# Kernel tuning notes

Measured on AMD Instinct MI355X. Metric: run time of the kernel, lower is better.

Reference implementation:

```python
import jax, jax.numpy as jnp
import numpy as np

N = 50000       # num nodes
E = 600000      # num edges
IN = 128        # in_channels
H = 4           # heads
C = 32          # out_channels per head
B = 3           # num bends (Bezier control points)
NEG_SLOPE = 0.2


def setup_inputs() -> dict:
    key = jax.random.key(0)
    ks = jax.random.split(key, 6)
    x = jax.random.normal(ks[0], (N, IN), dtype=jnp.float32)
    edge_index = jax.random.randint(ks[1], (2, E), 0, N)
    # Bezier coefficients at t=0.5 for a 3-point curve: [0.25, 0.5, 0.25]
    coeffs_t = jnp.array([0.25, 0.5, 0.25], dtype=jnp.float32)
    glorot_w = float(np.sqrt(2.0) * np.sqrt(6.0 / (H * C + IN)))
    glorot_a = float(np.sqrt(2.0) * np.sqrt(6.0 / (1 + C)))
    lin_weight = jax.random.uniform(ks[2], (B, H * C, IN), jnp.float32, -glorot_w, glorot_w)
    lin_bias = jnp.zeros((B, H * C), dtype=jnp.float32)
    att_src = jax.random.uniform(ks[3], (B, 1, H, C), jnp.float32, -glorot_a, glorot_a)
    att_dst = jax.random.uniform(ks[4], (B, 1, H, C), jnp.float32, -glorot_a, glorot_a)
    return {"x": x, "edge_index": edge_index, "coeffs_t": coeffs_t,
            "lin_weight": lin_weight, "lin_bias": lin_bias,
            "att_src": att_src, "att_dst": att_dst}


def reference(x, edge_index, coeffs_t, lin_weight, lin_bias, att_src, att_dst):
    # Bezier parameter interpolation: weighted sum over bends
    W = jnp.einsum('b,boi->oi', coeffs_t, lin_weight)      # [H*C, IN]
    bias = jnp.einsum('b,bo->o', coeffs_t, lin_bias)       # [H*C]
    a_src = jnp.einsum('b,bqhc->qhc', coeffs_t, att_src)   # [1,H,C]
    a_dst = jnp.einsum('b,bqhc->qhc', coeffs_t, att_dst)   # [1,H,C]

    n = x.shape[0]
    xt = (x @ W.T + bias).reshape(n, H, C)                 # [N,H,C]
    alpha_src = jnp.sum(xt * a_src, axis=-1)               # [N,H]
    alpha_dst = jnp.sum(xt * a_dst, axis=-1)               # [N,H]

    row, col = edge_index[0], edge_index[1]
    alpha = alpha_src[row] + alpha_dst[col]                # [E,H]
    alpha = jax.nn.leaky_relu(alpha, NEG_SLOPE)

    # scatter-softmax over incoming edges of each target node (col)
    amax = jax.ops.segment_max(alpha, col, num_segments=n)  # [N,H]
    ex = jnp.exp(alpha - amax[col])                         # [E,H]
    denom = jax.ops.segment_sum(ex, col, num_segments=n)    # [N,H]
    alpha = ex / (denom[col] + 1e-16)                       # [E,H]

    # weighted neighbor aggregation (edge-parallel segment reduction)
    msg = xt[row] * alpha[..., None]                        # [E,H,C]
    out = jax.ops.segment_sum(msg, col, num_segments=n)     # [N,H,C]
    return out.reshape(n, H * C)                            # concat=True
```

## Files before the change

### kernel.cpp

```cpp
#include <hip/hip_runtime.h>
#include <hip/hip_bf16.h>

#define GAT_IN   128
#define GAT_OUT  128
#define GAT_H    4
#define GAT_C    32
#define NEG_SLOPE 0.2f
#define BUCKET   48

typedef __attribute__((ext_vector_type(8))) short bf16x8;
typedef __attribute__((ext_vector_type(4))) float f32x4;
union U4 { uint4 u; bf16x8 v; };

static __device__ __forceinline__ unsigned int pack_bf16(float lo, float hi) {
    __hip_bfloat16 a = __float2bfloat16(lo);
    __hip_bfloat16 b = __float2bfloat16(hi);
    unsigned short ua = *reinterpret_cast<unsigned short*>(&a);
    unsigned short ub = *reinterpret_cast<unsigned short*>(&b);
    return (unsigned int)ua | ((unsigned int)ub << 16);
}

__global__ __launch_bounds__(256) void bucket_interp_kernel(
    const int* __restrict__ ei, int* __restrict__ cnt,
    unsigned short* __restrict__ esrc, int ne,
    const float* __restrict__ coeffs,
    const float* __restrict__ lw,
    const float* __restrict__ lb,
    const float* __restrict__ asr,
    const float* __restrict__ ads,
    unsigned int* __restrict__ wfrag,
    float* __restrict__ biasc,
    float* __restrict__ asrc, float* __restrict__ adst)
{
    int b = blockIdx.x;
    if (b < 32) {
        int i = b * 256 + threadIdx.x;
        float c0 = coeffs[0], c1 = coeffs[1], c2 = coeffs[2];
        int lane = (i >> 2) & 63;
        int nk   = i >> 8;
        int jw   = i & 3;
        int nt = nk >> 2, ks = nk & 3;
        int o = nt * 16 + (lane & 15);
        int k = ks * 32 + (lane >> 4) * 8 + jw * 2;
        int idx = o * 128 + k;
        float w0 = c0 * lw[idx]     + c1 * lw[16384 + idx]     + c2 * lw[32768 + idx];
        float w1 = c0 * lw[idx + 1] + c1 * lw[16384 + idx + 1] + c2 * lw[32768 + idx + 1];
        wfrag[i] = pack_bf16(w0, w1);
        if (b == 0 && threadIdx.x < 128) {
            int t = threadIdx.x;
            biasc[t] = c0 * lb[t]  + c1 * lb[128 + t]  + c2 * lb[256 + t];
            asrc[t]  = c0 * asr[t] + c1 * asr[128 + t] + c2 * asr[256 + t];
            adst[t]  = c0 * ads[t] + c1 * ads[128 + t] + c2 * ads[256 + t];
        }
        return;
    }
    int e = (b - 32) * 256 + threadIdx.x;
    if (e >= ne) return;
    int row = ei[e], col = ei[ne + e];
    int pos = atomicAdd(&cnt[col], 1);
    if (pos < BUCKET)
        esrc[(unsigned)col * BUCKET + pos] = (unsigned short)row;
}

__global__ __launch_bounds__(256) void gemm_alpha_kernel(
    const float* __restrict__ x,
    const unsigned int* __restrict__ wfrag,
    const float* __restrict__ biasc,
    const float* __restrict__ asrc,
    const float* __restrict__ adst,
    unsigned int* __restrict__ xtb,
    float* __restrict__ alpha_src,
    float* __restrict__ alpha_dst,
    int n)
{
    __shared__ __align__(16) float C[64 * 132];
    int tid  = threadIdx.x;
    int lane = tid & 63;
    int wave = tid >> 6;
    int quad = lane >> 4;
    int lm   = lane & 15;
    int m0   = blockIdx.x * 64 + wave * 16;

    f32x4 acc[8];
    #pragma unroll
    for (int t = 0; t < 8; ++t) acc[t] = (f32x4){0.f, 0.f, 0.f, 0.f};

    int arow = m0 + lm; if (arow >= n) arow = n - 1;
    const float4* xr = (const float4*)(x + (size_t)arow * 128 + quad * 8);
    const uint4*  wf = (const uint4*)wfrag;

    #pragma unroll
    for (int ks = 0; ks < 4; ++ks) {
        float4 a0 = xr[ks * 8 + 0];
        float4 a1 = xr[ks * 8 + 1];
        U4 af;
        af.u.x = pack_bf16(a0.x, a0.y);
        af.u.y = pack_bf16(a0.z, a0.w);
        af.u.z = pack_bf16(a1.x, a1.y);
        af.u.w = pack_bf16(a1.z, a1.w);
        #pragma unroll
        for (int nt = 0; nt < 8; ++nt) {
            U4 bf; bf.u = wf[(nt * 4 + ks) * 64 + lane];
            acc[nt] = __builtin_amdgcn_mfma_f32_16x16x32_bf16(
                af.v, bf.v, acc[nt], 0, 0, 0);
        }
    }

    #pragma unroll
    for (int nt = 0; nt < 8; ++nt) {
        int col = nt * 16 + lm;
        #pragma unroll
        for (int r = 0; r < 4; ++r) {
            int rowl = wave * 16 + quad * 4 + r;
            C[rowl * 132 + col] = acc[nt][r];
        }
    }
    __syncthreads();

    int rowl = wave * 16 + (lane >> 2);
    int seg  = lane & 3;
    int mrow = blockIdx.x * 64 + rowl;
    if (mrow < n) {
        const float4* cb = (const float4*)(C + rowl * 132 + seg * 32);
        const float4* bb = (const float4*)(biasc + seg * 32);
        const float4* sb = (const float4*)(asrc + seg * 32);
        const float4* db = (const float4*)(adst + seg * 32);
        float s = 0.f, d = 0.f;
        unsigned int ow[16];
        #pragma unroll
        for (int q = 0; q < 8; ++q) {
            float4 v = cb[q];
            float4 b = bb[q];
            v.x += b.x; v.y += b.y; v.z += b.z; v.w += b.w;
            float4 as = sb[q], ad = db[q];
            s += v.x * as.x + v.y * as.y + v.z * as.z + v.w * as.w;
            d += v.x * ad.x + v.y * ad.y + v.z * ad.z + v.w * ad.w;
            ow[q * 2 + 0] = pack_bf16(v.x, v.y);
            ow[q * 2 + 1] = pack_bf16(v.z, v.w);
        }
        alpha_src[mrow * 4 + seg] = s;
        alpha_dst[mrow * 4 + seg] = d;
        uint4* xo = (uint4*)(xtb + (size_t)mrow * 64 + seg * 16);
        #pragma unroll
        for (int q4 = 0; q4 < 4; ++q4)
            xo[q4] = make_uint4(ow[q4 * 4], ow[q4 * 4 + 1],
                                ow[q4 * 4 + 2], ow[q4 * 4 + 3]);
    }
}

static __device__ __forceinline__ void window16(
    uint4 qa, uint4 qb, int rem,
    unsigned int h, unsigned int sl, float ad,
    const unsigned int* __restrict__ xtb,
    const float* __restrict__ alpha_src,
    float& den, float4& acc)
{
    unsigned int w[8] = {qa.x, qa.y, qa.z, qa.w, qb.x, qb.y, qb.z, qb.w};
    int r[16];
    #pragma unroll
    for (int t = 0; t < 16; ++t) {
        unsigned int rr = (t & 1) ? (w[t >> 1] >> 16) : (w[t >> 1] & 0xFFFFu);
        r[t] = (t < rem) ? (int)rr : 0;
    }

    float as[16];
    #pragma unroll
    for (int t = 0; t < 16; ++t)
        as[t] = alpha_src[(((unsigned)r[t]) << 2) | h];
    uint2 u[16];
    #pragma unroll
    for (int t = 0; t < 16; ++t)
        u[t] = *(const uint2*)(xtb + ((((unsigned)r[t]) << 6) + (sl << 1)));

    float e[16];
    #pragma unroll
    for (int t = 0; t < 16; ++t) {
        float a = as[t] + ad;
        a = fmaxf(a, NEG_SLOPE * a);
        float ex = __expf(a);
        e[t] = (t < rem) ? ex : 0.f;
    }
    float s01 = e[0]+e[1],   s23 = e[2]+e[3],   s45 = e[4]+e[5],   s67 = e[6]+e[7];
    float s89 = e[8]+e[9],   sab = e[10]+e[11], scd = e[12]+e[13], sef = e[14]+e[15];
    den += ((s01+s23) + (s45+s67)) + ((s89+sab) + (scd+sef));

    #pragma unroll
    for (int t = 0; t < 16; ++t) {
        acc.x = fmaf(e[t], __uint_as_float(u[t].x << 16),          acc.x);
        acc.y = fmaf(e[t], __uint_as_float(u[t].x & 0xFFFF0000u),  acc.y);
        acc.z = fmaf(e[t], __uint_as_float(u[t].y << 16),          acc.z);
        acc.w = fmaf(e[t], __uint_as_float(u[t].y & 0xFFFF0000u),  acc.w);
    }
}

__global__ __launch_bounds__(256) void agg_kernel(
    const int* __restrict__ cnt,
    const unsigned short* __restrict__ esrc,
    const unsigned int* __restrict__ xtb,
    const float* __restrict__ alpha_src,
    const float* __restrict__ alpha_dst,
    float* __restrict__ out,
    int n)
{
    int wave = threadIdx.x >> 6;
    unsigned int lane = threadIdx.x & 63;
    unsigned int sub = lane >> 5;
    unsigned int sl  = lane & 31;
    int node = blockIdx.x * 8 + wave * 2 + (int)sub;
    bool active = node < n;
    int nodec = active ? node : 0;
    unsigned int h = sl >> 3;

    const uint4* ebq = (const uint4*)(esrc + (unsigned)nodec * BUCKET);
    uint4 qa = ebq[0];
    uint4 qb = ebq[1];
    int   m  = cnt[nodec];
    float ad = alpha_dst[((unsigned)nodec << 2) | h];
    if (!active) m = 0;
    if (m > BUCKET) m = BUCKET;

    float4 acc = make_float4(0.f, 0.f, 0.f, 0.f);
    float den = 0.f;

    window16(qa, qb, m, h, sl, ad, xtb, alpha_src, den, acc);

    for (int j = 16; j < m; j += 16) {
        int q = j >> 3;
        uint4 wa = ebq[q], wb = ebq[q + 1];
        window16(wa, wb, m - j, h, sl, ad, xtb, alpha_src, den, acc);
    }

    if (active) {
        float inv = 1.0f / (den + 1e-16f);
        ((float4*)out)[((unsigned)node << 5) | sl] =
            make_float4(acc.x * inv, acc.y * inv, acc.z * inv, acc.w * inv);
    }
}

extern "C" void kernel_launch(void* const* d_in, const int* in_sizes, int n_in,
                              void* d_out, int out_size, void* d_ws, size_t ws_size,
                              hipStream_t stream)
{
    const float* x      = (const float*)d_in[0];
    const int*   ei     = (const int*)  d_in[1];
    const float* coeffs = (const float*)d_in[2];
    const float* lw     = (const float*)d_in[3];
    const float* lb     = (const float*)d_in[4];
    const float* asr    = (const float*)d_in[5];
    const float* ads    = (const float*)d_in[6];
    float* out = (float*)d_out;

    int n  = in_sizes[0] / GAT_IN;
    int ne = in_sizes[1] / 2;

    float* ws        = (float*)d_ws;
    unsigned int* wfrag = (unsigned int*)ws;
    float* biasc     = ws + 16384;
    float* asrc      = ws + 16512;
    float* adst      = ws + 16640;
    unsigned int* xtb = (unsigned int*)(ws + 16768);
    float* alpha_src = (float*)(xtb + (size_t)n * 64);
    float* alpha_dst = alpha_src + (size_t)n * 4;
    int*   cnt       = (int*)(alpha_dst + (size_t)n * 4);
    unsigned short* esrc = (unsigned short*)(cnt + n);

    hipMemsetAsync(cnt, 0, (size_t)n * sizeof(int), stream);
    bucket_interp_kernel<<<32 + (ne + 255) / 256, 256, 0, stream>>>(
        ei, cnt, esrc, ne, coeffs, lw, lb, asr, ads, wfrag, biasc, asrc, adst);
    gemm_alpha_kernel<<<(n + 63) / 64, 256, 0, stream>>>(
        x, wfrag, biasc, asrc, adst, xtb, alpha_src, alpha_dst, n);
    agg_kernel<<<(n + 7) / 8, 256, 0, stream>>>(
        cnt, esrc, xtb, alpha_src, alpha_dst, out, n);
}
```

Measured before the change: 166.3 us.

## Partition edge bucketing by destination range per XCC with dynamic chunk stealing

Replaces the one-thread-per-edge bucketing with a persistent 2048-block grid. The destination-node range is split into 8 partitions, and each block starts on the partition matching its XCC id, so the atomics on cnt and the esrc writes for a given range tend to stay local to one die's L2. Blocks claim edge chunks dynamically through per-partition progress counters. In exchange, every block rescans the column array once per partition, eight reads of the edge column list in total, and pays extra syncthreads and atomic overhead per chunk.

```diff
diff --git a/kernel.cpp b/kernel.cpp
--- a/kernel.cpp
+++ b/kernel.cpp
@@ -7,6 +7,9 @@
 #define GAT_C    32
 #define NEG_SLOPE 0.2f
 #define BUCKET   48
+#define NPART    8
+#define EPT      8
+#define CHUNK    (256 * EPT)
 
 typedef __attribute__((ext_vector_type(8))) short bf16x8;
 typedef __attribute__((ext_vector_type(4))) float f32x4;
@@ -22,7 +25,8 @@
 
 __global__ __launch_bounds__(256) void bucket_interp_kernel(
     const int* __restrict__ ei, int* __restrict__ cnt,
-    unsigned short* __restrict__ esrc, int ne,
+    int* __restrict__ prog,
+    unsigned short* __restrict__ esrc, int ne, int n,
     const float* __restrict__ coeffs,
     const float* __restrict__ lw,
     const float* __restrict__ lb,
@@ -32,9 +36,9 @@
     float* __restrict__ biasc,
     float* __restrict__ asrc, float* __restrict__ adst)
 {
-    int b = blockIdx.x;
+    int b = blockIdx.x, tid = threadIdx.x;
     if (b < 32) {
-        int i = b * 256 + threadIdx.x;
+        int i = b * 256 + tid;
         float c0 = coeffs[0], c1 = coeffs[1], c2 = coeffs[2];
         int lane = (i >> 2) & 63;
         int nk   = i >> 8;
@@ -46,20 +50,49 @@
         float w0 = c0 * lw[idx]     + c1 * lw[16384 + idx]     + c2 * lw[32768 + idx];
         float w1 = c0 * lw[idx + 1] + c1 * lw[16384 + idx + 1] + c2 * lw[32768 + idx + 1];
         wfrag[i] = pack_bf16(w0, w1);
-        if (b == 0 && threadIdx.x < 128) {
-            int t = threadIdx.x;
-            biasc[t] = c0 * lb[t]  + c1 * lb[128 + t]  + c2 * lb[256 + t];
-            asrc[t]  = c0 * asr[t] + c1 * asr[128 + t] + c2 * asr[256 + t];
-            adst[t]  = c0 * ads[t] + c1 * ads[128 + t] + c2 * ads[256 + t];
-        }
-        return;
-    }
-    int e = (b - 32) * 256 + threadIdx.x;
-    if (e >= ne) return;
-    int row = ei[e], col = ei[ne + e];
-    int pos = atomicAdd(&cnt[col], 1);
-    if (pos < BUCKET)
-        esrc[(unsigned)col * BUCKET + pos] = (unsigned short)row;
+        if (b == 0 && tid < 128) {
+            biasc[tid] = c0 * lb[tid]  + c1 * lb[128 + tid]  + c2 * lb[256 + tid];
+            asrc[tid]  = c0 * asr[tid] + c1 * asr[128 + tid] + c2 * asr[256 + tid];
+            adst[tid]  = c0 * ads[tid] + c1 * ads[128 + tid] + c2 * ads[256 + tid];
+        }
+    }
+
+    unsigned int xcc;
+    asm volatile("s_getreg_b32 %0, hwreg(HW_REG_XCC_ID)" : "=s"(xcc));
+    xcc &= (NPART - 1);
+
+    __shared__ int s_chunk;
+    int pw = (n + NPART - 1) / NPART;
+    int nchunks = (ne + CHUNK - 1) / CHUNK;
+    const int* colp = ei + ne;
+
+    for (int pp = 0; pp < NPART; ++pp) {
+        int p  = ((int)xcc + pp) & (NPART - 1);
+        int lo = p * pw;
+        int hi = lo + pw; if (hi > n) hi = n;
+        while (true) {
+            __syncthreads();
+            if (tid == 0) s_chunk = atomicAdd(&prog[p], 1);
+            __syncthreads();
+            int c = s_chunk;
+            if (c >= nchunks) break;
+            int base = c * CHUNK + tid;
+            #pragma unroll
+            for (int i = 0; i < EPT; ++i) {
+                int e = base + i * 256;
+                if (e < ne) {
+                    int col = colp[e];
+                    if (col >= lo && col < hi) {
+                        int row = ei[e];
+                        int pos = atomicAdd(&cnt[col], 1);
+                        if (pos < BUCKET)
+                            esrc[(unsigned)col * BUCKET + pos] =
+                                (unsigned short)row;
+                    }
+                }
+            }
+        }
+    }
 }
 
 __global__ __launch_bounds__(256) void gemm_alpha_kernel(
@@ -262,11 +295,13 @@
     float* alpha_src = (float*)(xtb + (size_t)n * 64);
     float* alpha_dst = alpha_src + (size_t)n * 4;
     int*   cnt       = (int*)(alpha_dst + (size_t)n * 4);
-    unsigned short* esrc = (unsigned short*)(cnt + n);
-
-    hipMemsetAsync(cnt, 0, (size_t)n * sizeof(int), stream);
-    bucket_interp_kernel<<<32 + (ne + 255) / 256, 256, 0, stream>>>(
-        ei, cnt, esrc, ne, coeffs, lw, lb, asr, ads, wfrag, biasc, asrc, adst);
+    int*   prog      = cnt + n;
+    unsigned short* esrc = (unsigned short*)(prog + 16);
+
+    hipMemsetAsync(cnt, 0, (size_t)n * sizeof(int) + 64, stream);
+    bucket_interp_kernel<<<2048, 256, 0, stream>>>(
+        ei, cnt, prog, esrc, ne, n,
+        coeffs, lw, lb, asr, ads, wfrag, biasc, asrc, adst);
     gemm_alpha_kernel<<<(n + 63) / 64, 256, 0, stream>>>(
         x, wfrag, biasc, asrc, adst, xtb, alpha_src, alpha_dst, n);
     agg_kernel<<<(n + 7) / 8, 256, 0, stream>>>(
```

Result: slower. 367.4 us (+120.9%).

## Replace global-atomic edge bucketing with two-pass coarse/fine radix binning

Applied to the files above, without the earlier changes.

Edge bucketing by destination node is split into two passes. The first bins edges into coarse 256-node buckets using shared-memory histograms and one global atomic per bucket per block. The second builds each node's fixed-size source list in shared memory and writes it out with coalesced stores. This removes one scattered global atomic and one scattered 2-byte store per edge, as well as the memset of the count array, but it adds two kernel launches and an intermediate buffer with a fixed per-bucket capacity that could overflow on skewed inputs.

```diff
diff --git a/kernel.cpp b/kernel.cpp
--- a/kernel.cpp
+++ b/kernel.cpp
@@ -7,6 +7,10 @@
 #define GAT_C    32
 #define NEG_SLOPE 0.2f
 #define BUCKET   48
+#define NB       196
+#define CAP      4096
+#define E_B      4096
+#define EPTH     16
 
 typedef __attribute__((ext_vector_type(8))) short bf16x8;
 typedef __attribute__((ext_vector_type(4))) float f32x4;
@@ -20,9 +24,7 @@
     return (unsigned int)ua | ((unsigned int)ub << 16);
 }
 
-__global__ __launch_bounds__(256) void bucket_interp_kernel(
-    const int* __restrict__ ei, int* __restrict__ cnt,
-    unsigned short* __restrict__ esrc, int ne,
+__global__ __launch_bounds__(256) void interp_kernel(
     const float* __restrict__ coeffs,
     const float* __restrict__ lw,
     const float* __restrict__ lb,
@@ -30,36 +32,101 @@
     const float* __restrict__ ads,
     unsigned int* __restrict__ wfrag,
     float* __restrict__ biasc,
-    float* __restrict__ asrc, float* __restrict__ adst)
-{
-    int b = blockIdx.x;
-    if (b < 32) {
-        int i = b * 256 + threadIdx.x;
-        float c0 = coeffs[0], c1 = coeffs[1], c2 = coeffs[2];
-        int lane = (i >> 2) & 63;
-        int nk   = i >> 8;
-        int jw   = i & 3;
-        int nt = nk >> 2, ks = nk & 3;
-        int o = nt * 16 + (lane & 15);
-        int k = ks * 32 + (lane >> 4) * 8 + jw * 2;
-        int idx = o * 128 + k;
-        float w0 = c0 * lw[idx]     + c1 * lw[16384 + idx]     + c2 * lw[32768 + idx];
-        float w1 = c0 * lw[idx + 1] + c1 * lw[16384 + idx + 1] + c2 * lw[32768 + idx + 1];
-        wfrag[i] = pack_bf16(w0, w1);
-        if (b == 0 && threadIdx.x < 128) {
-            int t = threadIdx.x;
+    float* __restrict__ asrc, float* __restrict__ adst,
+    int* __restrict__ bucket_pos)
+{
+    int b = blockIdx.x, t = threadIdx.x;
+    int i = b * 256 + t;
+    float c0 = coeffs[0], c1 = coeffs[1], c2 = coeffs[2];
+    int lane = (i >> 2) & 63;
+    int nk   = i >> 8;
+    int jw   = i & 3;
+    int nt = nk >> 2, ks = nk & 3;
+    int o = nt * 16 + (lane & 15);
+    int k = ks * 32 + (lane >> 4) * 8 + jw * 2;
+    int idx = o * 128 + k;
+    float w0 = c0 * lw[idx]     + c1 * lw[16384 + idx]     + c2 * lw[32768 + idx];
+    float w1 = c0 * lw[idx + 1] + c1 * lw[16384 + idx + 1] + c2 * lw[32768 + idx + 1];
+    wfrag[i] = pack_bf16(w0, w1);
+    if (b == 0) {
+        if (t < 128) {
             biasc[t] = c0 * lb[t]  + c1 * lb[128 + t]  + c2 * lb[256 + t];
             asrc[t]  = c0 * asr[t] + c1 * asr[128 + t] + c2 * asr[256 + t];
             adst[t]  = c0 * ads[t] + c1 * ads[128 + t] + c2 * ads[256 + t];
         }
-        return;
-    }
-    int e = (b - 32) * 256 + threadIdx.x;
-    if (e >= ne) return;
-    int row = ei[e], col = ei[ne + e];
-    int pos = atomicAdd(&cnt[col], 1);
-    if (pos < BUCKET)
-        esrc[(unsigned)col * BUCKET + pos] = (unsigned short)row;
+        if (t < NB) bucket_pos[t] = 0;
+    }
+}
+
+__global__ __launch_bounds__(256) void pass1_kernel(
+    const int* __restrict__ ei, int ne,
+    int* __restrict__ bucket_pos,
+    unsigned int* __restrict__ coarse)
+{
+    __shared__ int hist[NB], hist2[NB], gbase[NB];
+    int tid = threadIdx.x;
+    int b0  = blockIdx.x * E_B;
+
+    for (int i = tid; i < NB; i += 256) { hist[i] = 0; hist2[i] = 0; }
+    __syncthreads();
+
+    int rows[EPTH], cols[EPTH];
+    #pragma unroll
+    for (int i = 0; i < EPTH; ++i) {
+        int e = b0 + i * 256 + tid;
+        if (e < ne) {
+            cols[i] = ei[ne + e];
+            rows[i] = ei[e];
+            atomicAdd(&hist[cols[i] >> 8], 1);
+        } else cols[i] = -1;
+    }
+    __syncthreads();
+
+    for (int i = tid; i < NB; i += 256)
+        gbase[i] = hist[i] ? atomicAdd(&bucket_pos[i], hist[i]) : 0;
+    __syncthreads();
+
+    #pragma unroll
+    for (int i = 0; i < EPTH; ++i) {
+        if (cols[i] >= 0) {
+            int bk  = cols[i] >> 8;
+            int pos = gbase[bk] + atomicAdd(&hist2[bk], 1);
+            if (pos < CAP)
+                coarse[bk * CAP + pos] =
+                    ((unsigned int)cols[i] << 16) | (unsigned int)rows[i];
+        }
+    }
+}
+
+__global__ __launch_bounds__(256) void pass2_kernel(
+    const int* __restrict__ bucket_pos,
+    const unsigned int* __restrict__ coarse,
+    int* __restrict__ cnt,
+    unsigned short* __restrict__ esrc,
+    int n)
+{
+    __shared__ __align__(16) unsigned short st[256 * BUCKET];
+    __shared__ int lcnt[256];
+    int b = blockIdx.x, tid = threadIdx.x;
+    lcnt[tid] = 0;
+    __syncthreads();
+
+    int cb = bucket_pos[b]; if (cb > CAP) cb = CAP;
+    for (int i = tid; i < cb; i += 256) {
+        unsigned int v = coarse[b * CAP + i];
+        int lc  = (int)(v >> 16) & 255;
+        int pos = atomicAdd(&lcnt[lc], 1);
+        if (pos < BUCKET)
+            st[lc * BUCKET + pos] = (unsigned short)(v & 0xFFFFu);
+    }
+    __syncthreads();
+
+    int nodes = n - b * 256; if (nodes > 256) nodes = 256;
+    if (tid < nodes) cnt[b * 256 + tid] = lcnt[tid];
+    int nq = nodes * 6;
+    uint4* dst = (uint4*)(esrc + (size_t)b * 256 * BUCKET);
+    const uint4* src = (const uint4*)st;
+    for (int i = tid; i < nq; i += 256) dst[i] = src[i];
 }
 
 __global__ __launch_bounds__(256) void gemm_alpha_kernel(
@@ -262,11 +329,15 @@
     float* alpha_src = (float*)(xtb + (size_t)n * 64);
     float* alpha_dst = alpha_src + (size_t)n * 4;
     int*   cnt       = (int*)(alpha_dst + (size_t)n * 4);
-    unsigned short* esrc = (unsigned short*)(cnt + n);
-
-    hipMemsetAsync(cnt, 0, (size_t)n * sizeof(int), stream);
-    bucket_interp_kernel<<<32 + (ne + 255) / 256, 256, 0, stream>>>(
-        ei, cnt, esrc, ne, coeffs, lw, lb, asr, ads, wfrag, biasc, asrc, adst);
+    int*   bucket_pos = cnt + n;
+    unsigned int* coarse = (unsigned int*)(bucket_pos + 256);
+    unsigned short* esrc = (unsigned short*)(coarse + (size_t)NB * CAP);
+
+    interp_kernel<<<32, 256, 0, stream>>>(
+        coeffs, lw, lb, asr, ads, wfrag, biasc, asrc, adst, bucket_pos);
+    pass1_kernel<<<(ne + E_B - 1) / E_B, 256, 0, stream>>>(
+        ei, ne, bucket_pos, coarse);
+    pass2_kernel<<<NB, 256, 0, stream>>>(bucket_pos, coarse, cnt, esrc, n);
     gemm_alpha_kernel<<<(n + 63) / 64, 256, 0, stream>>>(
         x, wfrag, biasc, asrc, adst, xtb, alpha_src, alpha_dst, n);
     agg_kernel<<<(n + 7) / 8, 256, 0, stream>>>(
```

Result: faster. 152.6 us (-8.2%).
